# Optimization experiments

Hardware: AMD Instinct MI355X
Metric: run time of the kernel (lower is better)

The kernel has to match this reference:

```python
import jax, jax.numpy as jnp
import numpy as np

B, N_FED, INPUT_DIM, LATENT_DIM = 8192, 16384, 1024, 512


def setup_inputs() -> dict:
    key = jax.random.key(0)
    k1, k2, k3 = jax.random.split(key, 3)
    enc = jax.random.normal(k1, (B, LATENT_DIM), dtype=jnp.float32)
    X_fed = jax.random.normal(k2, (N_FED, INPUT_DIM), dtype=jnp.float32)
    # torch.rand -> uniform [0, 1)
    domain_diff = jax.random.uniform(k3, (INPUT_DIM, LATENT_DIM), dtype=jnp.float32)
    return {"enc": enc, "X_fed": X_fed, "domain_diff": domain_diff}


def reference(enc, X_fed, domain_diff):
    # K = V = X_fed @ domain_diff  (computed once; torch source computes it twice)
    kv = X_fed @ domain_diff                      # (N_fed, latent)
    scores = jnp.einsum('bd,nd->bn', enc, kv) / enc.shape[1]  # scale by latent_dim
    attn = jax.nn.softmax(scores, axis=1)         # softmax over N_fed axis
    z = attn @ kv                                 # (B, latent)
    return z
```

## Files before the change

### kernel.cpp

```cpp
#include <hip/hip_runtime.h>
#include <hip/hip_bf16.h>
#include <stdint.h>

#define ENC_B 8192
#define NFED  16384
#define INDIM 1024
#define LAT   512
#define SCALE (1.0f/512.0f)

typedef __attribute__((ext_vector_type(4))) float f32x4;
typedef __attribute__((ext_vector_type(8))) short short8;
typedef __attribute__((ext_vector_type(4))) short short4_t;

static __device__ __forceinline__ short f2bf(float x){
  union { float f; uint32_t u; } v; v.f = x;
  uint32_t r = v.u + 0x7FFFu + ((v.u >> 16) & 1u);
  return (short)(r >> 16);
}
static __device__ __forceinline__ float bf2f(short s){
  union { float f; uint32_t u; } v; v.u = ((uint32_t)(unsigned short)s) << 16; return v.f;
}

static __device__ __forceinline__ void gload16(const void* g, void* l){
  __builtin_amdgcn_global_load_lds(
      (const __attribute__((address_space(1))) void*)g,
      (__attribute__((address_space(3))) void*)l, 16, 0, 0);
}

__global__ void ddT_kernel(const float* __restrict__ dd, short* __restrict__ ddT){
  const int n = blockIdx.x;
  for (int k = threadIdx.x; k < INDIM; k += 256)
    ddT[(size_t)n*INDIM + k] = f2bf(dd[(size_t)k*LAT + n]);
}

__global__ __launch_bounds__(256) void encb_kernel(const float* __restrict__ enc,
                                                   short* __restrict__ encb){
  const int gid = blockIdx.x*256 + threadIdx.x;
  const size_t base = (size_t)gid * 8;
  float4 v0 = *(const float4*)(enc + base);
  float4 v1 = *(const float4*)(enc + base + 4);
  short8 s;
  s[0]=f2bf(v0.x*SCALE); s[1]=f2bf(v0.y*SCALE); s[2]=f2bf(v0.z*SCALE); s[3]=f2bf(v0.w*SCALE);
  s[4]=f2bf(v1.x*SCALE); s[5]=f2bf(v1.y*SCALE); s[6]=f2bf(v1.z*SCALE); s[7]=f2bf(v1.w*SCALE);
  *(short8*)(encb + base) = s;
}

__global__ __launch_bounds__(256, 2) void kv_gemm_kernel(const float* __restrict__ X,
                                                         const short* __restrict__ ddT,
                                                         short* __restrict__ kv){
  __shared__ __align__(16) short As[128*40];
  __shared__ __align__(16) short Bs[128*40];
  const int t = threadIdx.x;
  const int lane = t & 63, w = t >> 6;
  const int lr = lane & 15, lg = lane >> 4;
  const int m0 = (blockIdx.x >> 2) * 128;
  const int n0 = (blockIdx.x & 3) * 128;
  const int wm = (w >> 1) * 64, wn = (w & 1) * 64;
  f32x4 acc[4][4];
  #pragma unroll
  for (int i=0;i<4;++i)
    #pragma unroll
    for (int j=0;j<4;++j) acc[i][j] = (f32x4){0.f,0.f,0.f,0.f};

  for (int k0 = 0; k0 < INDIM; k0 += 32) {
    #pragma unroll
    for (int i = 0; i < 4; ++i) {
      int idx = t + i*256;
      int row = idx >> 3, c4 = (idx & 7)*4;
      float4 v = *(const float4*)(X + (size_t)(m0+row)*INDIM + k0 + c4);
      short4_t s; s[0]=f2bf(v.x); s[1]=f2bf(v.y); s[2]=f2bf(v.z); s[3]=f2bf(v.w);
      *(short4_t*)(As + row*40 + c4) = s;
    }
    #pragma unroll
    for (int i = 0; i < 2; ++i) {
      int idx = t + i*256;
      int row = idx >> 2, c8 = (idx & 3)*8;
      *(uint4*)(Bs + row*40 + c8) = *(const uint4*)(ddT + (size_t)(n0+row)*INDIM + k0 + c8);
    }
    __syncthreads();
    short8 a[4], b[4];
    #pragma unroll
    for (int i=0;i<4;++i) a[i] = *(short8*)(As + (wm + i*16 + lr)*40 + lg*8);
    #pragma unroll
    for (int i=0;i<4;++i) b[i] = *(short8*)(Bs + (wn + i*16 + lr)*40 + lg*8);
    #pragma unroll
    for (int i=0;i<4;++i)
      #pragma unroll
      for (int j=0;j<4;++j)
        acc[i][j] = __builtin_amdgcn_mfma_f32_16x16x32_bf16(a[i], b[j], acc[i][j], 0,0,0);
    __syncthreads();
  }
  #pragma unroll
  for (int i=0;i<4;++i)
    #pragma unroll
    for (int j=0;j<4;++j)
      #pragma unroll
      for (int r=0;r<4;++r)
        kv[(size_t)(m0 + wm + i*16 + lg*4 + r)*LAT + n0 + wn + j*16 + lr] = f2bf(acc[i][j][r]);
}

__global__ __launch_bounds__(256) void kvT_kernel(const short* __restrict__ kv,
                                                  short* __restrict__ kvT){
  __shared__ short tile[64][72];
  const int t = threadIdx.x;
  const int bn = blockIdx.x & (NFED/64 - 1);
  const int bd = blockIdx.x / (NFED/64);
  #pragma unroll
  for (int i=0;i<2;++i){
    int idx = t + i*256; int row = idx >> 3, cc = (idx & 7)*8;
    *(uint4*)&tile[row][cc] = *(const uint4*)(kv + (size_t)(bn*64+row)*LAT + bd*64 + cc);
  }
  __syncthreads();
  #pragma unroll
  for (int i=0;i<2;++i){
    int idx = t + i*256; int drow = idx >> 3, nn = (idx & 7)*8;
    short8 v;
    #pragma unroll
    for (int j=0;j<8;++j) v[j] = tile[nn+j][drow];
    *(short8*)(kvT + (size_t)(bd*64+drow)*NFED + bn*64 + nn) = v;
  }
}

__global__ __launch_bounds__(256, 4) void s_gemm_kernel(const short* __restrict__ encb,
                                                        const short* __restrict__ kv,
                                                        short* __restrict__ Pc,
                                                        float* __restrict__ lpart,
                                                        int cbase, int chunk){
  __shared__ __align__(16) char lds[32768 + 512];
  short* As = (short*)lds;
  short* Bs = (short*)(lds + 16384);
  const int t = threadIdx.x;
  const int lane = t & 63, w = t >> 6;
  const int lr = lane & 15, lg = lane >> 4;
  const int n0g = cbase + blockIdx.x * 128;
  const int m0  = blockIdx.y * 128;

  const short* asrc[4]; const short* bsrc[4];
  #pragma unroll
  for (int i=0;i<4;++i){
    int ca = i*256 + w*64 + lane;
    int row = ca >> 3;
    int kcs = (lane & 7) ^ (row & 7);
    asrc[i] = kv   + (size_t)(n0g + row)*LAT + kcs*8;
    bsrc[i] = encb + (size_t)(m0  + row)*LAT + kcs*8;
  }

  f32x4 acc[2][8];
  #pragma unroll
  for (int i=0;i<2;++i)
    #pragma unroll
    for (int j=0;j<8;++j) acc[i][j] = (f32x4){0.f,0.f,0.f,0.f};

  for (int ks = 0; ks < 8; ++ks){
    #pragma unroll
    for (int i=0;i<4;++i){
      gload16(asrc[i], (char*)As + i*4096 + w*1024);
      gload16(bsrc[i], (char*)Bs + i*4096 + w*1024);
      asrc[i] += 64; bsrc[i] += 64;
    }
    __syncthreads();

    #pragma unroll
    for (int kk=0;kk<2;++kk){
      const uint32_t kbyte = (uint32_t)(kk*64 + lg*16);
      short8 b[2];
      #pragma unroll
      for (int ri=0;ri<2;++ri){
        int row = w*32 + ri*16 + lr;
        b[ri] = *(short8*)((char*)Bs + row*128 + (kbyte ^ ((uint32_t)(row & 7) << 4)));
      }
      #pragma unroll
      for (int h=0;h<2;++h){
        short8 a[4];
        #pragma unroll
        for (int j=0;j<4;++j){
          int row = (h*4 + j)*16 + lr;
          a[j] = *(short8*)((char*)As + row*128 + (kbyte ^ ((uint32_t)(row & 7) << 4)));
        }
        #pragma unroll
        for (int ri=0;ri<2;++ri)
          #pragma unroll
          for (int j=0;j<4;++j)
            acc[ri][h*4+j] = __builtin_amdgcn_mfma_f32_16x16x32_bf16(a[j], b[ri], acc[ri][h*4+j], 0,0,0);
      }
    }
    __syncthreads();
  }

  char*  Pt   = lds;
  float* lsum = (float*)(lds + 32768);
  #pragma unroll
  for (int ri=0;ri<2;++ri){
    const int q = w*32 + ri*16 + lr;
    const uint32_t rswz = ((uint32_t)(q & 7)) << 4;
    float ps = 0.f;
    #pragma unroll
    for (int dj=0;dj<8;++dj){
      short4_t pv;
      #pragma unroll
      for (int r=0;r<4;++r){
        float pe = __expf(acc[ri][dj][r]);
        ps += pe;
        pv[r] = f2bf(pe);
      }
      *(short4_t*)(Pt + q*256 + (((uint32_t)(dj*32 + lg*8)) ^ rswz)) = pv;
    }
    ps += __shfl_xor(ps, 16, 64);
    ps += __shfl_xor(ps, 32, 64);
    if (lg == 0) lsum[q] = ps;
  }
  __syncthreads();
  #pragma unroll
  for (int i=0;i<8;++i){
    uint32_t c = (uint32_t)(i*256 + t);
    uint32_t row = c >> 4, c16 = c & 15;
    short8 v = *(short8*)(Pt + row*256 + ((c16*16) ^ (((uint32_t)(row & 7)) << 4)));
    *(short8*)(Pc + (size_t)(m0 + row)*chunk + blockIdx.x*128 + c16*8) = v;
  }
  if (t < 128){
    int jsl = (cbase >> 7) + blockIdx.x;
    lpart[(size_t)jsl*ENC_B + m0 + t] = lsum[t];
  }
}

__global__ __launch_bounds__(256, 4) void z_gemm_kernel(const short* __restrict__ kvT,
                                                        const short* __restrict__ Pc,
                                                        short* __restrict__ zb,
                                                        int cbase, int chunk,
                                                        int sliceBase, int first){
  __shared__ __align__(16) short As[64*64];
  __shared__ __align__(16) short Bs[128*64];
  const int t = threadIdx.x;
  const int lane = t & 63, w = t >> 6;
  const int lr = lane & 15, lg = lane >> 4;
  const int n0 = blockIdx.x * 128;
  const int m0 = blockIdx.y * 64;
  const int s  = blockIdx.z;
  const int sl = sliceBase + s;
  const int klocal0 = s * (chunk >> 1);

  const short* Asrc[2];
  #pragma unroll
  for (int i=0;i<2;++i){
    int ca = i*256 + w*64 + lane;
    int row = ca >> 3;
    int kcs = (lane & 7) ^ (row & 7);
    Asrc[i] = kvT + (size_t)(m0 + row)*NFED + cbase + klocal0 + kcs*8;
  }
  const short* Bsrc[4];
  #pragma unroll
  for (int i=0;i<4;++i){
    int ca = i*256 + w*64 + lane;
    int row = ca >> 3;
    int kcs = (lane & 7) ^ (row & 7);
    Bsrc[i] = Pc + (size_t)(n0 + row)*chunk + klocal0 + kcs*8;
  }

  f32x4 acc[2][4];
  #pragma unroll
  for (int i=0;i<2;++i)
    #pragma unroll
    for (int j=0;j<4;++j) acc[i][j] = (f32x4){0.f,0.f,0.f,0.f};

  const int ksteps = chunk >> 7;
  for (int ks = 0; ks < ksteps; ++ks) {
    #pragma unroll
    for (int i=0;i<2;++i){
      gload16(Asrc[i], (char*)As + i*4096 + w*1024);
      Asrc[i] += 64;
    }
    #pragma unroll
    for (int i=0;i<4;++i){
      gload16(Bsrc[i], (char*)Bs + i*4096 + w*1024);
      Bsrc[i] += 64;
    }
    __syncthreads();

    #pragma unroll
    for (int kk=0;kk<2;++kk){
      const uint32_t kbyte = kk*64 + lg*16;
      short8 a[4], b[2];
      #pragma unroll
      for (int dj=0;dj<4;++dj){
        int row = dj*16 + lr;
        a[dj] = *(short8*)((char*)As + row*128 + (kbyte ^ ((uint32_t)(row & 7) << 4)));
      }
      #pragma unroll
      for (int ri=0;ri<2;++ri){
        int row = w*32 + ri*16 + lr;
        b[ri] = *(short8*)((char*)Bs + row*128 + (kbyte ^ ((uint32_t)(row & 7) << 4)));
      }
      #pragma unroll
      for (int ri=0;ri<2;++ri)
        #pragma unroll
        for (int dj=0;dj<4;++dj)
          acc[ri][dj] = __builtin_amdgcn_mfma_f32_16x16x32_bf16(a[dj], b[ri], acc[ri][dj], 0,0,0);
    }
    __syncthreads();
  }

  #pragma unroll
  for (int ri=0;ri<2;++ri)
    #pragma unroll
    for (int dj=0;dj<4;++dj)
      #pragma unroll
      for (int r=0;r<4;++r) {
        int d    = m0 + dj*16 + lg*4 + r;
        int rowq = n0 + w*32 + ri*16 + lr;
        size_t idx = ((size_t)sl*LAT + d)*ENC_B + rowq;
        float v = acc[ri][dj][r];
        if (!first) v += bf2f(zb[idx]);
        zb[idx] = f2bf(v);
      }
}

__global__ __launch_bounds__(256) void lred_kernel(const float* __restrict__ lpart,
                                                   float* __restrict__ linv){
  const int row = blockIdx.x*256 + threadIdx.x;
  float sum = 0.f;
  for (int j = 0; j < NFED/128; ++j)
    sum += lpart[(size_t)j*ENC_B + row];
  linv[row] = 1.0f / sum;
}

__global__ __launch_bounds__(256) void zcomb_kernel(const short* __restrict__ zb,
                                                    const float* __restrict__ linv,
                                                    float* __restrict__ out){
  __shared__ float tile[64][65];
  const int t = threadIdx.x;
  const int bx = blockIdx.x;
  const int by = blockIdx.y;
  #pragma unroll
  for (int i=0;i<4;++i){
    int idx = t + i*256;
    int dr = idx >> 4, rc = (idx & 15)*4;
    float s0=0.f, s1=0.f, s2=0.f, s3=0.f;
    #pragma unroll
    for (int sl=0; sl<8; ++sl){
      short4_t v = *(const short4_t*)(zb + ((size_t)sl*LAT + by*64 + dr)*ENC_B + bx*64 + rc);
      s0 += bf2f(v[0]); s1 += bf2f(v[1]); s2 += bf2f(v[2]); s3 += bf2f(v[3]);
    }
    tile[dr][rc+0]=s0; tile[dr][rc+1]=s1; tile[dr][rc+2]=s2; tile[dr][rc+3]=s3;
  }
  __syncthreads();
  #pragma unroll
  for (int i=0;i<4;++i){
    int idx = t + i*256;
    int rr = idx >> 4, dc = (idx & 15)*4;
    float li = linv[bx*64 + rr];
    float4 o;
    o.x = tile[dc+0][rr]*li; o.y = tile[dc+1][rr]*li;
    o.z = tile[dc+2][rr]*li; o.w = tile[dc+3][rr]*li;
    *(float4*)(out + (size_t)(bx*64+rr)*LAT + by*64 + dc) = o;
  }
}

extern "C" void kernel_launch(void* const* d_in, const int* in_sizes, int n_in,
                              void* d_out, int out_size, void* d_ws, size_t ws_size,
                              hipStream_t stream) {
  const float* enc = (const float*)d_in[0];
  const float* X   = (const float*)d_in[1];
  const float* dd  = (const float*)d_in[2];
  float* out = (float*)d_out;

  short* kvb   = (short*)d_ws;
  short* kvT   = (short*)((char*)d_ws + 16777216);
  short* encb  = (short*)((char*)d_ws + 33554432);
  float* lpart = (float*)((char*)d_ws + 41943040);
  short* ddT   = (short*)((char*)d_ws + 41943040);
  float* linv  = (float*)((char*)d_ws + 46137344);
  short* zb    = (short*)((char*)d_ws + 50331648);
  short* Pc    = (short*)((char*)d_ws + 117440512);

  int chunk;
  if      (ws_size >= (size_t)117440512 + (size_t)4096*ENC_B*2) chunk = 4096;
  else if (ws_size >= (size_t)117440512 + (size_t)2048*ENC_B*2) chunk = 2048;
  else                                                          chunk = 1024;

  ddT_kernel<<<LAT, 256, 0, stream>>>(dd, ddT);
  kv_gemm_kernel<<<(NFED/128)*(LAT/128), 256, 0, stream>>>(X, ddT, kvb);
  kvT_kernel<<<(NFED/64)*(LAT/64), 256, 0, stream>>>(kvb, kvT);
  encb_kernel<<<ENC_B*LAT/(256*8), 256, 0, stream>>>(enc, encb);

  const int nc = NFED / chunk;
  for (int c = 0; c < nc; ++c) {
    s_gemm_kernel<<<dim3(chunk/128, ENC_B/128), 256, 0, stream>>>(
        encb, kvb, Pc, lpart, c*chunk, chunk);
    z_gemm_kernel<<<dim3(ENC_B/128, LAT/64, 2), 256, 0, stream>>>(
        kvT, Pc, zb, c*chunk, chunk, (c & 3)*2, (c < 4) ? 1 : 0);
  }
  lred_kernel<<<ENC_B/256, 256, 0, stream>>>(lpart, linv);
  zcomb_kernel<<<dim3(ENC_B/64, LAT/64), 256, 0, stream>>>(zb, linv, out);
}
```

Baseline: 416.7 us.

## Rewrite KV GEMM with direct global-to-LDS loads, swizzled LDS and coalesced stores

The X @ domain_diff GEMM now loads tiles with global_load_lds straight into XOR-swizzled shared memory, keeping X as fp32 in LDS and converting it to bf16 at fragment-read time. Operand roles, warp tiling and occupancy (launch bounds 4) change as well. The output is staged through LDS so rows are written to kv with 16-byte coalesced stores. The aim is to cut register-staged load overhead, bank conflicts and scattered 2-byte global stores, at the cost of extra LDS traffic and repeated conversion work.

```diff
diff --git a/kernel.cpp b/kernel.cpp
--- a/kernel.cpp
+++ b/kernel.cpp
@@ -45,58 +45,105 @@
   *(short8*)(encb + base) = s;
 }
 
-__global__ __launch_bounds__(256, 2) void kv_gemm_kernel(const float* __restrict__ X,
+__global__ __launch_bounds__(256, 4) void kv_gemm_kernel(const float* __restrict__ X,
                                                          const short* __restrict__ ddT,
                                                          short* __restrict__ kv){
-  __shared__ __align__(16) short As[128*40];
-  __shared__ __align__(16) short Bs[128*40];
+  __shared__ __align__(16) char lds[32768 + 512];
+  short* As = (short*)lds;
+  float* Bs = (float*)(lds + 8192);
   const int t = threadIdx.x;
   const int lane = t & 63, w = t >> 6;
   const int lr = lane & 15, lg = lane >> 4;
-  const int m0 = (blockIdx.x >> 2) * 128;
-  const int n0 = (blockIdx.x & 3) * 128;
-  const int wm = (w >> 1) * 64, wn = (w & 1) * 64;
-  f32x4 acc[4][4];
-  #pragma unroll
-  for (int i=0;i<4;++i)
-    #pragma unroll
-    for (int j=0;j<4;++j) acc[i][j] = (f32x4){0.f,0.f,0.f,0.f};
-
-  for (int k0 = 0; k0 < INDIM; k0 += 32) {
-    #pragma unroll
-    for (int i = 0; i < 4; ++i) {
-      int idx = t + i*256;
-      int row = idx >> 3, c4 = (idx & 7)*4;
-      float4 v = *(const float4*)(X + (size_t)(m0+row)*INDIM + k0 + c4);
-      short4_t s; s[0]=f2bf(v.x); s[1]=f2bf(v.y); s[2]=f2bf(v.z); s[3]=f2bf(v.w);
-      *(short4_t*)(As + row*40 + c4) = s;
-    }
-    #pragma unroll
-    for (int i = 0; i < 2; ++i) {
-      int idx = t + i*256;
-      int row = idx >> 2, c8 = (idx & 3)*8;
-      *(uint4*)(Bs + row*40 + c8) = *(const uint4*)(ddT + (size_t)(n0+row)*INDIM + k0 + c8);
-    }
-    __syncthreads();
-    short8 a[4], b[4];
-    #pragma unroll
-    for (int i=0;i<4;++i) a[i] = *(short8*)(As + (wm + i*16 + lr)*40 + lg*8);
-    #pragma unroll
-    for (int i=0;i<4;++i) b[i] = *(short8*)(Bs + (wn + i*16 + lr)*40 + lg*8);
-    #pragma unroll
-    for (int i=0;i<4;++i)
-      #pragma unroll
-      for (int j=0;j<4;++j)
-        acc[i][j] = __builtin_amdgcn_mfma_f32_16x16x32_bf16(a[i], b[j], acc[i][j], 0,0,0);
-    __syncthreads();
-  }
-  #pragma unroll
-  for (int i=0;i<4;++i)
-    #pragma unroll
-    for (int j=0;j<4;++j)
-      #pragma unroll
-      for (int r=0;r<4;++r)
-        kv[(size_t)(m0 + wm + i*16 + lg*4 + r)*LAT + n0 + wn + j*16 + lr] = f2bf(acc[i][j][r]);
+  const int n0 = blockIdx.x * 128;
+  const int m0 = blockIdx.y * 128;
+
+  const short* asrc[2];
+  #pragma unroll
+  for (int i=0;i<2;++i){
+    int ca = i*256 + w*64 + lane;
+    int row = ca >> 2;
+    int c  = (lane & 3) ^ (row & 3) ^ ((row >> 2) & 3);
+    asrc[i] = ddT + (size_t)(n0 + row)*INDIM + c*8;
+  }
+  const float* bsrc[4];
+  #pragma unroll
+  for (int i=0;i<4;++i){
+    int ca = i*256 + w*64 + lane;
+    int row = ca >> 3;
+    int c  = (lane & 7) ^ (row & 7);
+    bsrc[i] = X + (size_t)(m0 + row)*INDIM + c*4;
+  }
+
+  f32x4 acc[2][8];
+  #pragma unroll
+  for (int i=0;i<2;++i)
+    #pragma unroll
+    for (int j=0;j<8;++j) acc[i][j] = (f32x4){0.f,0.f,0.f,0.f};
+
+  for (int ks = 0; ks < 32; ++ks){
+    #pragma unroll
+    for (int i=0;i<2;++i){
+      gload16(asrc[i], (char*)As + i*4096 + w*1024);
+      asrc[i] += 32;
+    }
+    #pragma unroll
+    for (int i=0;i<4;++i){
+      gload16(bsrc[i], (char*)Bs + i*4096 + w*1024);
+      bsrc[i] += 32;
+    }
+    __syncthreads();
+
+    short8 b[2];
+    #pragma unroll
+    for (int ri=0;ri<2;++ri){
+      int row = w*32 + ri*16 + lr;
+      uint32_t sw = ((uint32_t)(row & 7)) << 4;
+      f32x4 f0 = *(const f32x4*)((char*)Bs + row*128 + ((uint32_t)(lg*32) ^ sw));
+      f32x4 f1 = *(const f32x4*)((char*)Bs + row*128 + ((uint32_t)(lg*32 + 16) ^ sw));
+      short8 s;
+      s[0]=f2bf(f0[0]); s[1]=f2bf(f0[1]); s[2]=f2bf(f0[2]); s[3]=f2bf(f0[3]);
+      s[4]=f2bf(f1[0]); s[5]=f2bf(f1[1]); s[6]=f2bf(f1[2]); s[7]=f2bf(f1[3]);
+      b[ri] = s;
+    }
+    #pragma unroll
+    for (int h=0;h<2;++h){
+      short8 a[4];
+      #pragma unroll
+      for (int j=0;j<4;++j){
+        int row = (h*4 + j)*16 + lr;
+        uint32_t c = (uint32_t)(lg ^ (row & 3) ^ ((row >> 2) & 3));
+        a[j] = *(short8*)((char*)As + row*64 + c*16);
+      }
+      #pragma unroll
+      for (int ri=0;ri<2;++ri)
+        #pragma unroll
+        for (int j=0;j<4;++j)
+          acc[ri][h*4+j] = __builtin_amdgcn_mfma_f32_16x16x32_bf16(a[j], b[ri], acc[ri][h*4+j], 0,0,0);
+    }
+    __syncthreads();
+  }
+
+  char* Pt = lds;
+  #pragma unroll
+  for (int ri=0;ri<2;++ri){
+    const int m = w*32 + ri*16 + lr;
+    const uint32_t rswz = ((uint32_t)(m & 7)) << 4;
+    #pragma unroll
+    for (int dj=0;dj<8;++dj){
+      short4_t pv;
+      #pragma unroll
+      for (int r=0;r<4;++r) pv[r] = f2bf(acc[ri][dj][r]);
+      *(short4_t*)(Pt + m*256 + (((uint32_t)(dj*32 + lg*8)) ^ rswz)) = pv;
+    }
+  }
+  __syncthreads();
+  #pragma unroll
+  for (int i=0;i<8;++i){
+    uint32_t c = (uint32_t)(i*256 + t);
+    uint32_t row = c >> 4, c16 = c & 15;
+    short8 v = *(short8*)(Pt + row*256 + ((c16*16) ^ (((uint32_t)(row & 7)) << 4)));
+    *(short8*)(kv + (size_t)(m0 + row)*LAT + n0 + c16*8) = v;
+  }
 }
 
 __global__ __launch_bounds__(256) void kvT_kernel(const short* __restrict__ kv,
@@ -378,7 +425,7 @@
   else                                                          chunk = 1024;
 
   ddT_kernel<<<LAT, 256, 0, stream>>>(dd, ddT);
-  kv_gemm_kernel<<<(NFED/128)*(LAT/128), 256, 0, stream>>>(X, ddT, kvb);
+  kv_gemm_kernel<<<dim3(LAT/128, NFED/128), 256, 0, stream>>>(X, ddT, kvb);
   kvT_kernel<<<(NFED/64)*(LAT/64), 256, 0, stream>>>(kvb, kvT);
   encb_kernel<<<ENC_B*LAT/(256*8), 256, 0, stream>>>(enc, encb);
 
```

New measurement: 417.9 us. No clear change (+0.3%).
